# Performance work log

Measured on AMD Instinct MI355X. Metric: run time of the kernel, lower is better.

## Reference

```python
import jax, jax.numpy as jnp
import numpy as np

LN_EPS = 1e-5  # torch LayerNorm default
ITERS = 3

def _ln(x, g, b):
    m = jnp.mean(x, -1, keepdims=True)
    v = jnp.var(x, -1, keepdims=True)
    return (x - m) * jax.lax.rsqrt(v + LN_EPS) * g + b

def setup_inputs() -> dict:
    key = jax.random.key(0)
    ks = jax.random.split(key, 10)
    B, N, D, S, H = 32, 4096, 256, 8, 512
    sc = D ** -0.5
    w = lambda k, shape, s: jax.random.normal(k, shape, jnp.float32) * s
    return {
        "inputs": w(ks[0], (B, N, D), 1.0),
        "noise": w(ks[1], (B, S, D), 1.0),
        "ln_in_g": jnp.ones((D,), jnp.float32), "ln_in_b": jnp.zeros((D,), jnp.float32),
        "ln_slot_g": jnp.ones((D,), jnp.float32), "ln_slot_b": jnp.zeros((D,), jnp.float32),
        "ln_mlp_g": jnp.ones((D,), jnp.float32), "ln_mlp_b": jnp.zeros((D,), jnp.float32),
        "slot_mu": jnp.zeros((1, 1, D), jnp.float32),
        "slot_sigma": jnp.ones((1, 1, D), jnp.float32),
        "Wq": w(ks[2], (D, D), sc), "Wk": w(ks[3], (D, D), sc), "Wv": w(ks[4], (D, D), sc),
        "W_ih": w(ks[5], (D, 3 * D), sc), "W_hh": w(ks[6], (D, 3 * D), sc),
        "b_ih": jnp.zeros((3 * D,), jnp.float32), "b_hh": jnp.zeros((3 * D,), jnp.float32),
        "W1": w(ks[7], (D, H), sc), "b1": jnp.zeros((H,), jnp.float32),
        "W2": w(ks[8], (H, D), H ** -0.5), "b2": jnp.zeros((D,), jnp.float32),
    }

def reference(inputs, noise, ln_in_g, ln_in_b, ln_slot_g, ln_slot_b, ln_mlp_g, ln_mlp_b,
              slot_mu, slot_sigma, Wq, Wk, Wv, W_ih, W_hh, b_ih, b_hh, W1, b1, W2, b2):
    b, n, d = inputs.shape
    scale = d ** -0.5
    x = _ln(inputs, ln_in_g, ln_in_b)
    sigma = jnp.clip(jax.nn.softplus(slot_sigma), 0.1, 2.0)
    slots = slot_mu + sigma * noise            # [b, S, d]
    k = x @ Wk                                  # [b, n, d]
    v = x @ Wv                                  # [b, n, d]
    for _ in range(ITERS):
        slots_prev = slots
        s = _ln(slots, ln_slot_g, ln_slot_b)
        q = s @ Wq                              # [b, S, d]
        dots = jnp.einsum('bnd,bsd->bns', k, q) * scale
        attn = jax.nn.softmax(dots, axis=1)     # softmax over inputs (dim=1), as in source
        updates = jnp.einsum('bns,bnd->bsd', attn, v)
        # torch GRUCell: gate order (reset, update, new)
        gx = updates @ W_ih + b_ih
        gh = slots_prev @ W_hh + b_hh
        xr, xz, xn = jnp.split(gx, 3, -1)
        hr, hz, hn = jnp.split(gh, 3, -1)
        r = jax.nn.sigmoid(xr + hr)
        z = jax.nn.sigmoid(xz + hz)
        ng = jnp.tanh(xn + r * hn)
        slots = (1.0 - z) * ng + z * slots_prev
        m = _ln(slots, ln_mlp_g, ln_mlp_b)
        slots = slots + (jax.nn.relu(m @ W1 + b1) @ W2 + b2)
    return slots
```

## Files before the change

kernel.cpp:

```cpp
#include <hip/hip_runtime.h>

typedef unsigned short u16;
typedef unsigned int u32;
typedef short bf16x8 __attribute__((ext_vector_type(8)));
typedef float f32x4 __attribute__((ext_vector_type(4)));

#define DEV static __device__ __forceinline__

constexpr int CH = 16;
constexpr int NB = 4096 / CH;
constexpr float LN_EPS = 1e-5f;
constexpr float SCALE = 0.0625f;

DEV float bf2f(u32 u) { return __uint_as_float(u << 16); }
DEV float bfe(short x) { return __uint_as_float(((u32)(u16)x) << 16); }
DEV u16 f2bf(float f) {
  u32 u = __float_as_uint(f);
  return (u16)((u + 0x7fffu + ((u >> 16) & 1u)) >> 16);
}
DEV u32 pk2(float a, float b) { return (u32)f2bf(a) | ((u32)f2bf(b) << 16); }


__global__ __launch_bounds__(256) void k_convert(
    const float* __restrict__ Wk, const float* __restrict__ Wv,
    const float* __restrict__ Wih, const float* __restrict__ Whh,
    const float* __restrict__ W1, const float* __restrict__ W2,
    const float* __restrict__ Wq,
    u16* __restrict__ wkvT, u16* __restrict__ wih_f, u16* __restrict__ whh_f,
    u16* __restrict__ w1_f, u16* __restrict__ w2_f, u16* __restrict__ wq_f,
    u16* __restrict__ wqt) {
  int idx = blockIdx.x * 256 + threadIdx.x;
  if (idx < 131072) {
    int n = idx >> 8, k = idx & 255;
    float v = (n < 256) ? Wk[k * 256 + n] : Wv[k * 256 + (n - 256)];
    wkvT[idx] = f2bf(v);
    return;
  }
  idx -= 131072;
  if (idx < 196608) {
    int j = idx & 7, lane = (idx >> 3) & 63, tile = idx >> 9;
    int kt = tile & 7, nt = tile >> 3;
    int k = kt * 32 + ((lane >> 4) << 3) + j, n = nt * 16 + (lane & 15);
    wih_f[idx] = f2bf(Wih[k * 768 + n]);
    return;
  }
  idx -= 196608;
  if (idx < 196608) {
    int j = idx & 7, lane = (idx >> 3) & 63, tile = idx >> 9;
    int kt = tile & 7, nt = tile >> 3;
    int k = kt * 32 + ((lane >> 4) << 3) + j, n = nt * 16 + (lane & 15);
    whh_f[idx] = f2bf(Whh[k * 768 + n]);
    return;
  }
  idx -= 196608;
  if (idx < 131072) {
    int j = idx & 7, lane = (idx >> 3) & 63, tile = idx >> 9;
    int kt = tile & 7, nt = tile >> 3;
    int k = kt * 32 + ((lane >> 4) << 3) + j, n = nt * 16 + (lane & 15);
    w1_f[idx] = f2bf(W1[k * 512 + n]);
    return;
  }
  idx -= 131072;
  if (idx < 131072) {
    int j = idx & 7, lane = (idx >> 3) & 63, tile = idx >> 9;
    int kt = tile & 15, nt = tile >> 4;
    int k = kt * 32 + ((lane >> 4) << 3) + j, n = nt * 16 + (lane & 15);
    w2_f[idx] = f2bf(W2[k * 256 + n]);
    return;
  }
  idx -= 131072;
  if (idx < 65536) {
    int j = idx & 7, lane = (idx >> 3) & 63, tile = idx >> 9;
    int kt = tile & 7, nt = tile >> 3;
    int k = kt * 32 + ((lane >> 4) << 3) + j, n = nt * 16 + (lane & 15);
    wq_f[idx] = f2bf(Wq[k * 256 + n]);
    return;
  }
  idx -= 65536;
  if (idx < 65536) {
    int t = idx >> 8, d = idx & 255;
    wqt[idx] = f2bf(Wq[d * 256 + t]);
    return;
  }
}

__global__ __launch_bounds__(256) void k_ln(const float* __restrict__ in,
    const float* __restrict__ g, const float* __restrict__ b,
    u16* __restrict__ xbf) {
  int row = blockIdx.x * 4 + (threadIdx.x >> 6);
  int lane = threadIdx.x & 63;
  float4 v = ((const float4*)(in + (size_t)row * 256))[lane];
  float s = v.x + v.y + v.z + v.w;
  float ss = v.x * v.x + v.y * v.y + v.z * v.z + v.w * v.w;
#pragma unroll
  for (int o = 32; o; o >>= 1) { s += __shfl_xor(s, o); ss += __shfl_xor(ss, o); }
  float mean = s * (1.f / 256.f);
  float rstd = rsqrtf(ss * (1.f / 256.f) - mean * mean + LN_EPS);
  float4 gv = ((const float4*)g)[lane];
  float4 bv = ((const float4*)b)[lane];
  uint2 o;
  o.x = pk2((v.x - mean) * rstd * gv.x + bv.x, (v.y - mean) * rstd * gv.y + bv.y);
  o.y = pk2((v.z - mean) * rstd * gv.z + bv.z, (v.w - mean) * rstd * gv.w + bv.w);
  ((uint2*)(xbf + (size_t)row * 256))[lane] = o;
}

__global__ __launch_bounds__(256) void k_slots_init(
    const float* __restrict__ noise, const float* __restrict__ mu,
    const float* __restrict__ sig, const float* __restrict__ g,
    const float* __restrict__ b, const u16* __restrict__ wqt,
    float* __restrict__ slots, float* __restrict__ qbuf) {
  int bs = blockIdx.x, t = threadIdx.x;
  float sg = sig[t];
  float sp = (sg > 20.f) ? sg : log1pf(expf(sg));
  sp = fminf(fmaxf(sp, 0.1f), 2.0f);
  float sl = mu[t] + sp * noise[bs * 256 + t];
  slots[bs * 256 + t] = sl;
  __shared__ float red[8];
  __shared__ __align__(16) float sln[256];
  float s = sl, ss = sl * sl;
#pragma unroll
  for (int o = 32; o; o >>= 1) { s += __shfl_xor(s, o); ss += __shfl_xor(ss, o); }
  int w = t >> 6;
  if ((t & 63) == 0) { red[w] = s; red[4 + w] = ss; }
  __syncthreads();
  s = red[0] + red[1] + red[2] + red[3];
  ss = red[4] + red[5] + red[6] + red[7];
  float mean = s * (1.f / 256.f);
  float rstd = rsqrtf(ss * (1.f / 256.f) - mean * mean + LN_EPS);
  sln[t] = (sl - mean) * rstd * g[t] + b[t];
  __syncthreads();
  float acc = 0.f;
  const bf16x8* wqp = (const bf16x8*)(wqt + t * 256);
#pragma unroll 4
  for (int db = 0; db < 32; ++db) {
    float q8[8];
    *(float4*)q8 = *(const float4*)&sln[db * 8];
    *(float4*)(q8 + 4) = *(const float4*)&sln[db * 8 + 4];
    bf16x8 wv = wqp[db];
#pragma unroll
    for (int j = 0; j < 8; ++j) acc += q8[j] * bfe(wv[j]);
  }
  qbuf[bs * 256 + t] = acc;
}

__global__ __launch_bounds__(256) void k_gemm(
    const u16* __restrict__ X, const u16* __restrict__ Wt,
    u16* __restrict__ kT, u16* __restrict__ Vv) {
  __shared__ u16 smem[16896];
  int bid = blockIdx.x;
  int mt = bid >> 2, nt = bid & 3;
  int w = threadIdx.x >> 6, lane = threadIdx.x & 63;
  int wr = w >> 1, wc = w & 1;
  f32x4 acc[4][4] = {};
  for (int ks = 0; ks < 4; ++ks) {
#pragma unroll
    for (int i = 0; i < 4; ++i) {
      int cbase = (w * 4 + i) * 64;
      int c = cbase + lane;
      int r = c >> 3;
      int swz = (c & 7) ^ (r & 7);
      const u16* srcA = X + (mt * 128 + r) * 256 + ks * 64 + swz * 8;
      const u16* srcB = Wt + (nt * 128 + r) * 256 + ks * 64 + swz * 8;
      __builtin_amdgcn_global_load_lds(
          (const __attribute__((address_space(1))) void*)srcA,
          (__attribute__((address_space(3))) void*)(smem + cbase * 8), 16, 0, 0);
      __builtin_amdgcn_global_load_lds(
          (const __attribute__((address_space(1))) void*)srcB,
          (__attribute__((address_space(3))) void*)(smem + 8192 + cbase * 8), 16, 0, 0);
    }
    __syncthreads();
#pragma unroll
    for (int kk = 0; kk < 2; ++kk) {
      bf16x8 af[4], bfr[4];
#pragma unroll
      for (int m = 0; m < 4; ++m) {
        int lrow = wr * 64 + m * 16 + (lane & 15);
        int slot = (kk * 4 + (lane >> 4)) ^ (lrow & 7);
        af[m] = *(const bf16x8*)((const char*)smem + lrow * 128 + slot * 16);
      }
#pragma unroll
      for (int n = 0; n < 4; ++n) {
        int lcol = wc * 64 + n * 16 + (lane & 15);
        int slot = (kk * 4 + (lane >> 4)) ^ (lcol & 7);
        bfr[n] = *(const bf16x8*)((const char*)smem + 16384 + lcol * 128 + slot * 16);
      }
#pragma unroll
      for (int m = 0; m < 4; ++m)
#pragma unroll
        for (int n = 0; n < 4; ++n)
          acc[m][n] = __builtin_amdgcn_mfma_f32_16x16x32_bf16(af[m], bfr[n], acc[m][n], 0, 0, 0);
    }
    __syncthreads();
  }
  int bb = (mt * 128) >> 12;
  int nb0 = (mt * 128) & 4095;
  if (nt < 2) {
#pragma unroll
    for (int m = 0; m < 4; ++m)
#pragma unroll
      for (int n = 0; n < 4; ++n) {
        int col = wc * 64 + n * 16 + (lane & 15);
        int r0 = wr * 64 + m * 16 + (lane >> 4) * 4;
        uint2 pk;
        pk.x = pk2(acc[m][n][0], acc[m][n][1]);
        pk.y = pk2(acc[m][n][2], acc[m][n][3]);
        *(uint2*)((char*)smem + col * 264 + r0 * 2) = pk;
      }
    __syncthreads();
    u16* outp = kT + bb * (1 << 20) + nt * 128 * 4096 + nb0;
    for (int i = 0; i < 32; ++i) {
      int dl = w * 32 + i;
      u32 val = *(const u32*)((const char*)smem + dl * 264 + lane * 4);
      *(u32*)(outp + dl * 4096 + 2 * lane) = val;
    }
  } else {
#pragma unroll
    for (int m = 0; m < 4; ++m)
#pragma unroll
      for (int n = 0; n < 4; ++n) {
        int col = wc * 64 + n * 16 + (lane & 15);
        int r0 = wr * 64 + m * 16 + (lane >> 4) * 4;
#pragma unroll
        for (int j = 0; j < 4; ++j)
          *((u16*)((char*)smem + (r0 + j) * 264 + col * 2)) = f2bf(acc[m][n][j]);
      }
    __syncthreads();
    u16* outp = Vv + (mt * 128) * 256 + (nt - 2) * 128;
    for (int i = 0; i < 32; ++i) {
      int nl = w * 32 + i;
      u32 val = *(const u32*)((const char*)smem + nl * 264 + lane * 4);
      *(u32*)(outp + nl * 256 + 2 * lane) = val;
    }
  }
}

__global__ __launch_bounds__(128) void k_attn(
    const u16* __restrict__ kT, const u16* __restrict__ Vv,
    const float* __restrict__ qbuf,
    float* __restrict__ part_ml, float* __restrict__ part_upd) {
  int b = blockIdx.x >> 4, c = blockIdx.x & 15;
  int n0 = c * NB;
  int t = threadIdx.x;
  int w = t >> 6, lane = t & 63;
  __shared__ __align__(16) float qT[256][8];
  __shared__ __align__(16) float pl[NB][8];
  __shared__ float red[16];
  for (int i = t; i < 2048; i += 128) {
    int s = i >> 8, d = i & 255;
    qT[d][s] = qbuf[(b * 8 + s) * 256 + d];
  }
  __syncthreads();
  float acc[8][2] = {};
  const u16* kp = kT + b * (1 << 20) + n0 + 2 * t;
#pragma unroll 8
  for (int d = 0; d < 256; ++d) {
    u32 kk = *(const u32*)(kp + d * 4096);
    float k0 = bf2f(kk & 0xffffu), k1 = bf2f(kk >> 16);
    float q8[8];
    *(float4*)q8 = *(const float4*)&qT[d][0];
    *(float4*)(q8 + 4) = *(const float4*)&qT[d][4];
#pragma unroll
    for (int s = 0; s < 8; ++s) { acc[s][0] += k0 * q8[s]; acc[s][1] += k1 * q8[s]; }
  }
  float mx[8];
#pragma unroll
  for (int s = 0; s < 8; ++s) {
    acc[s][0] *= SCALE; acc[s][1] *= SCALE;
    float lm = fmaxf(acc[s][0], acc[s][1]);
#pragma unroll
    for (int o = 32; o; o >>= 1) lm = fmaxf(lm, __shfl_xor(lm, o));
    if (lane == 0) red[w * 8 + s] = lm;
  }
  __syncthreads();
#pragma unroll
  for (int s = 0; s < 8; ++s) mx[s] = fmaxf(red[s], red[8 + s]);
  __syncthreads();
#pragma unroll
  for (int s = 0; s < 8; ++s) {
    float p0 = __expf(acc[s][0] - mx[s]);
    float p1 = __expf(acc[s][1] - mx[s]);
    pl[2 * t][s] = p0; pl[2 * t + 1][s] = p1;
    float l = p0 + p1;
#pragma unroll
    for (int o = 32; o; o >>= 1) l += __shfl_xor(l, o);
    if (lane == 0) red[w * 8 + s] = l;
  }
  __syncthreads();
  if (t < 8) {
    part_ml[(b * 16 + c) * 16 + t] = mx[t];
    part_ml[(b * 16 + c) * 16 + 8 + t] = red[t] + red[8 + t];
  }
  float upd[8][2] = {};
  const u16* vp = Vv + (b * 4096 + n0) * 256 + 2 * t;
#pragma unroll 4
  for (int n = 0; n < NB; ++n) {
    u32 vv = *(const u32*)(vp + n * 256);
    float v0 = bf2f(vv & 0xffffu), v1 = bf2f(vv >> 16);
    float p8[8];
    *(float4*)p8 = *(const float4*)&pl[n][0];
    *(float4*)(p8 + 4) = *(const float4*)&pl[n][4];
#pragma unroll
    for (int s = 0; s < 8; ++s) { upd[s][0] += p8[s] * v0; upd[s][1] += p8[s] * v1; }
  }
  float* up = part_upd + ((b * 16 + c) * 8) * 256 + 2 * t;
#pragma unroll
  for (int s = 0; s < 8; ++s) {
    float2 o2; o2.x = upd[s][0]; o2.y = upd[s][1];
    *(float2*)(up + s * 256) = o2;
  }
}

__global__ __launch_bounds__(256) void k_comb(
    const float* __restrict__ pml, const float* __restrict__ pupd,
    const float* __restrict__ slots_in,
    u16* __restrict__ ufrag, u16* __restrict__ hfrag) {
  int w = threadIdx.x >> 6, lane = threadIdx.x & 63;
  int row = blockIdx.x * 4 + w;
  int b = row >> 3, s = row & 7;
  float mv[16], lv[16], M = -1e30f;
#pragma unroll
  for (int c = 0; c < 16; ++c) {
    mv[c] = pml[(b * 16 + c) * 16 + s];
    lv[c] = pml[(b * 16 + c) * 16 + 8 + s];
    M = fmaxf(M, mv[c]);
  }
  float L = 0.f;
#pragma unroll
  for (int c = 0; c < 16; ++c) { mv[c] = __expf(mv[c] - M); L += lv[c] * mv[c]; }
  float inv = 1.f / L;
  int d0 = lane * 4;
  float4 acc = {0.f, 0.f, 0.f, 0.f};
#pragma unroll
  for (int c = 0; c < 16; ++c) {
    float4 p = *(const float4*)(pupd + (size_t)((b * 16 + c) * 8 + s) * 256 + d0);
    float wc = mv[c] * inv;
    acc.x += wc * p.x; acc.y += wc * p.y; acc.z += wc * p.z; acc.w += wc * p.w;
  }
  int mt = row >> 4, kt = d0 >> 5;
  int laneA = ((d0 >> 3) & 3) * 16 + (row & 15);
  int j0 = d0 & 7;
  uint2 pk;
  pk.x = pk2(acc.x, acc.y); pk.y = pk2(acc.z, acc.w);
  *(uint2*)(ufrag + ((mt * 8 + kt) * 64 + laneA) * 8 + j0) = pk;
  float4 hv = *(const float4*)(slots_in + row * 256 + d0);
  pk.x = pk2(hv.x, hv.y); pk.y = pk2(hv.z, hv.w);
  *(uint2*)(hfrag + ((mt * 8 + kt) * 64 + laneA) * 8 + j0) = pk;
}

__global__ __launch_bounds__(256) void k_gru(
    const u16* __restrict__ ufrag, const u16* __restrict__ hfrag,
    const u16* __restrict__ wih_f, const u16* __restrict__ whh_f,
    const float* __restrict__ bih, const float* __restrict__ bhh,
    const float* __restrict__ slots_in, float* __restrict__ snew) {
  int w = threadIdx.x >> 6, lane = threadIdx.x & 63;
  int unit = blockIdx.x * 4 + w;
  int mt = unit >> 4, g = unit & 15;
  const bf16x8* wih = (const bf16x8*)wih_f;
  const bf16x8* whh = (const bf16x8*)whh_f;
  f32x4 ar = {}, az = {}, an = {}, hr = {}, hz = {}, hn = {};
#pragma unroll
  for (int kt = 0; kt < 8; ++kt) {
    bf16x8 au = *(const bf16x8*)(ufrag + ((mt * 8 + kt) * 64 + lane) * 8);
    bf16x8 ah = *(const bf16x8*)(hfrag + ((mt * 8 + kt) * 64 + lane) * 8);
    ar = __builtin_amdgcn_mfma_f32_16x16x32_bf16(au, wih[(g * 8 + kt) * 64 + lane], ar, 0, 0, 0);
    az = __builtin_amdgcn_mfma_f32_16x16x32_bf16(au, wih[((16 + g) * 8 + kt) * 64 + lane], az, 0, 0, 0);
    an = __builtin_amdgcn_mfma_f32_16x16x32_bf16(au, wih[((32 + g) * 8 + kt) * 64 + lane], an, 0, 0, 0);
    hr = __builtin_amdgcn_mfma_f32_16x16x32_bf16(ah, whh[(g * 8 + kt) * 64 + lane], hr, 0, 0, 0);
    hz = __builtin_amdgcn_mfma_f32_16x16x32_bf16(ah, whh[((16 + g) * 8 + kt) * 64 + lane], hz, 0, 0, 0);
    hn = __builtin_amdgcn_mfma_f32_16x16x32_bf16(ah, whh[((32 + g) * 8 + kt) * 64 + lane], hn, 0, 0, 0);
  }
  int t = g * 16 + (lane & 15);
  float cr = bih[t], cz = bih[256 + t], cn = bih[512 + t];
  float dr = bhh[t], dz = bhh[256 + t], dn = bhh[512 + t];
#pragma unroll
  for (int j = 0; j < 4; ++j) {
    int row = mt * 16 + (lane >> 4) * 4 + j;
    float r = 1.f / (1.f + __expf(-(ar[j] + cr + hr[j] + dr)));
    float z = 1.f / (1.f + __expf(-(az[j] + cz + hz[j] + dz)));
    float ng = tanhf(an[j] + cn + r * (hn[j] + dn));
    float h = slots_in[row * 256 + t];
    snew[row * 256 + t] = (1.f - z) * ng + z * h;
  }
}

__global__ __launch_bounds__(256) void k_rowln(
    const float* __restrict__ xin, const float* __restrict__ g,
    const float* __restrict__ bb, u16* __restrict__ frag) {
  int w = threadIdx.x >> 6, lane = threadIdx.x & 63;
  int row = blockIdx.x * 4 + w;
  int d0 = lane * 4;
  float4 v = *(const float4*)(xin + row * 256 + d0);
  float s = v.x + v.y + v.z + v.w;
  float ss = v.x * v.x + v.y * v.y + v.z * v.z + v.w * v.w;
#pragma unroll
  for (int o = 32; o; o >>= 1) { s += __shfl_xor(s, o); ss += __shfl_xor(ss, o); }
  float mean = s * (1.f / 256.f);
  float rstd = rsqrtf(ss * (1.f / 256.f) - mean * mean + LN_EPS);
  float4 gv = *(const float4*)(g + d0);
  float4 bv = *(const float4*)(bb + d0);
  float o0 = (v.x - mean) * rstd * gv.x + bv.x;
  float o1 = (v.y - mean) * rstd * gv.y + bv.y;
  float o2 = (v.z - mean) * rstd * gv.z + bv.z;
  float o3 = (v.w - mean) * rstd * gv.w + bv.w;
  int mt = row >> 4, kt = d0 >> 5;
  int laneA = ((d0 >> 3) & 3) * 16 + (row & 15);
  int j0 = d0 & 7;
  uint2 pk;
  pk.x = pk2(o0, o1); pk.y = pk2(o2, o3);
  *(uint2*)(frag + ((mt * 8 + kt) * 64 + laneA) * 8 + j0) = pk;
}

__global__ __launch_bounds__(256) void k_mlp1(
    const u16* __restrict__ mfrag, const u16* __restrict__ w1_f,
    const float* __restrict__ b1v, u16* __restrict__ h1frag) {
  int w = threadIdx.x >> 6, lane = threadIdx.x & 63;
  int unit = blockIdx.x * 4 + w;
  int mt = unit >> 5, nt = unit & 31;
  const bf16x8* bw = (const bf16x8*)w1_f;
  f32x4 acc = {};
#pragma unroll
  for (int kt = 0; kt < 8; ++kt)
    acc = __builtin_amdgcn_mfma_f32_16x16x32_bf16(
        *(const bf16x8*)(mfrag + ((mt * 8 + kt) * 64 + lane) * 8),
        bw[(nt * 8 + kt) * 64 + lane], acc, 0, 0, 0);
  int col = nt * 16 + (lane & 15);
  float bbv = b1v[col];
  int kt2 = col >> 5;
  int j2 = col & 7;
  int laneBase = ((col >> 3) & 3) * 16;
#pragma unroll
  for (int j = 0; j < 4; ++j) {
    int row = mt * 16 + (lane >> 4) * 4 + j;
    float vv = fmaxf(acc[j] + bbv, 0.f);
    h1frag[((mt * 16 + kt2) * 64 + laneBase + (row & 15)) * 8 + j2] = f2bf(vv);
  }
}

__global__ __launch_bounds__(256) void k_mlp2(
    const u16* __restrict__ h1frag, const u16* __restrict__ w2_f,
    const float* __restrict__ b2v, const float* __restrict__ snew,
    float* __restrict__ sout) {
  int w = threadIdx.x >> 6, lane = threadIdx.x & 63;
  int unit = blockIdx.x * 4 + w;
  int mt = unit >> 4, nt = unit & 15;
  const bf16x8* bw = (const bf16x8*)w2_f;
  f32x4 acc = {};
#pragma unroll
  for (int kt = 0; kt < 16; ++kt)
    acc = __builtin_amdgcn_mfma_f32_16x16x32_bf16(
        *(const bf16x8*)(h1frag + ((mt * 16 + kt) * 64 + lane) * 8),
        bw[(nt * 16 + kt) * 64 + lane], acc, 0, 0, 0);
  int col = nt * 16 + (lane & 15);
  float bbv = b2v[col];
#pragma unroll
  for (int j = 0; j < 4; ++j) {
    int row = mt * 16 + (lane >> 4) * 4 + j;
    sout[row * 256 + col] = acc[j] + bbv + snew[row * 256 + col];
  }
}

__global__ __launch_bounds__(256) void k_q(
    const u16* __restrict__ slfrag, const u16* __restrict__ wq_f,
    float* __restrict__ qbuf) {
  int w = threadIdx.x >> 6, lane = threadIdx.x & 63;
  int unit = blockIdx.x * 4 + w;
  int mt = unit >> 4, nt = unit & 15;
  const bf16x8* bw = (const bf16x8*)wq_f;
  f32x4 acc = {};
#pragma unroll
  for (int kt = 0; kt < 8; ++kt)
    acc = __builtin_amdgcn_mfma_f32_16x16x32_bf16(
        *(const bf16x8*)(slfrag + ((mt * 8 + kt) * 64 + lane) * 8),
        bw[(nt * 8 + kt) * 64 + lane], acc, 0, 0, 0);
  int col = nt * 16 + (lane & 15);
#pragma unroll
  for (int j = 0; j < 4; ++j) {
    int row = mt * 16 + (lane >> 4) * 4 + j;
    qbuf[row * 256 + col] = acc[j];
  }
}

extern "C" void kernel_launch(void* const* d_in, const int* in_sizes, int n_in,
                              void* d_out, int out_size, void* d_ws, size_t ws_size,
                              hipStream_t stream) {
  (void)in_sizes; (void)n_in; (void)out_size; (void)ws_size;
  const float* inputs    = (const float*)d_in[0];
  const float* noise     = (const float*)d_in[1];
  const float* ln_in_g   = (const float*)d_in[2];
  const float* ln_in_b   = (const float*)d_in[3];
  const float* ln_slot_g = (const float*)d_in[4];
  const float* ln_slot_b = (const float*)d_in[5];
  const float* ln_mlp_g  = (const float*)d_in[6];
  const float* ln_mlp_b  = (const float*)d_in[7];
  const float* slot_mu   = (const float*)d_in[8];
  const float* slot_sig  = (const float*)d_in[9];
  const float* Wq        = (const float*)d_in[10];
  const float* Wk        = (const float*)d_in[11];
  const float* Wv        = (const float*)d_in[12];
  const float* W_ih      = (const float*)d_in[13];
  const float* W_hh      = (const float*)d_in[14];
  const float* b_ih      = (const float*)d_in[15];
  const float* b_hh      = (const float*)d_in[16];
  const float* W1        = (const float*)d_in[17];
  const float* b1        = (const float*)d_in[18];
  const float* W2        = (const float*)d_in[19];
  const float* b2        = (const float*)d_in[20];

  char* p = (char*)d_ws;
  auto take = [&](size_t bytes) { char* r = p; p += (bytes + 255) & ~(size_t)255; return r; };
  u16* xbf      = (u16*)take((size_t)131072 * 256 * 2);
  u16* kT       = (u16*)take((size_t)32 * 256 * 4096 * 2);
  u16* Vv       = (u16*)take((size_t)32 * 4096 * 256 * 2);
  u16* wkvT     = (u16*)take(131072 * 2);
  u16* wih_f    = (u16*)take(196608 * 2);
  u16* whh_f    = (u16*)take(196608 * 2);
  u16* w1_f     = (u16*)take(131072 * 2);
  u16* w2_f     = (u16*)take(131072 * 2);
  u16* wq_f     = (u16*)take(65536 * 2);
  u16* wqt      = (u16*)take(65536 * 2);
  u16* ufrag    = (u16*)take(65536 * 2);
  u16* hfrag    = (u16*)take(65536 * 2);
  u16* mfrag    = (u16*)take(65536 * 2);
  u16* slfrag   = (u16*)take(65536 * 2);
  u16* h1frag   = (u16*)take(131072 * 2);
  float* snew   = (float*)take(65536 * 4);
  float* slotsA = (float*)take(256 * 256 * 4);
  float* slotsB = (float*)take(256 * 256 * 4);
  float* qbuf   = (float*)take(256 * 256 * 4);
  float* pml    = (float*)take(32 * 16 * 16 * 4);
  float* pupd   = (float*)take((size_t)32 * 16 * 8 * 256 * 4);

  k_convert<<<3584, 256, 0, stream>>>(Wk, Wv, W_ih, W_hh, W1, W2, Wq,
                                      wkvT, wih_f, whh_f, w1_f, w2_f, wq_f, wqt);
  k_ln<<<32768, 256, 0, stream>>>(inputs, ln_in_g, ln_in_b, xbf);
  k_slots_init<<<256, 256, 0, stream>>>(noise, slot_mu, slot_sig, ln_slot_g, ln_slot_b, wqt, slotsA, qbuf);
  k_gemm<<<4096, 256, 0, stream>>>(xbf, wkvT, kT, Vv);

  const float* scur = slotsA;
  for (int it = 0; it < 3; ++it) {
    k_attn<<<512, 128, 0, stream>>>(kT, Vv, qbuf, pml, pupd);
    k_comb<<<64, 256, 0, stream>>>(pml, pupd, scur, ufrag, hfrag);
    k_gru<<<64, 256, 0, stream>>>(ufrag, hfrag, wih_f, whh_f, b_ih, b_hh, scur, snew);
    k_rowln<<<64, 256, 0, stream>>>(snew, ln_mlp_g, ln_mlp_b, mfrag);
    k_mlp1<<<128, 256, 0, stream>>>(mfrag, w1_f, b1, h1frag);
    float* sout = (it == 2) ? (float*)d_out : ((it == 0) ? slotsB : slotsA);
    k_mlp2<<<64, 256, 0, stream>>>(h1frag, w2_f, b2, snew, sout);
    if (it < 2) {
      k_rowln<<<64, 256, 0, stream>>>(sout, ln_slot_g, ln_slot_b, slfrag);
      k_q<<<64, 256, 0, stream>>>(slfrag, wq_f, qbuf);
    }
    scur = sout;
  }
}
```

Baseline: 324.7 us.

## Fuse LayerNorms into the K/V GEMM, MLP1 and Q projection kernels

The input LayerNorm is computed inside the K/V GEMM. Each block normalizes its 128 fp32 rows straight into swizzled LDS, so the separate k_ln pass and the bf16 xbf buffer in global memory go away. The per-iteration row LayerNorms before MLP1 and the Q projection are likewise folded into those GEMM kernels through shared-memory fragments, which removes four small launches per loop. The trade-offs: the fp32 input is now read once per N-tile (four times per row block), the larger LDS footprint may cut occupancy, and weight tiles are loaded after each barrier with no double buffering.

```diff
diff --git a/kernel.cpp b/kernel.cpp
--- a/kernel.cpp
+++ b/kernel.cpp
@@ -82,26 +82,6 @@
     wqt[idx] = f2bf(Wq[d * 256 + t]);
     return;
   }
-}
-
-__global__ __launch_bounds__(256) void k_ln(const float* __restrict__ in,
-    const float* __restrict__ g, const float* __restrict__ b,
-    u16* __restrict__ xbf) {
-  int row = blockIdx.x * 4 + (threadIdx.x >> 6);
-  int lane = threadIdx.x & 63;
-  float4 v = ((const float4*)(in + (size_t)row * 256))[lane];
-  float s = v.x + v.y + v.z + v.w;
-  float ss = v.x * v.x + v.y * v.y + v.z * v.z + v.w * v.w;
-#pragma unroll
-  for (int o = 32; o; o >>= 1) { s += __shfl_xor(s, o); ss += __shfl_xor(ss, o); }
-  float mean = s * (1.f / 256.f);
-  float rstd = rsqrtf(ss * (1.f / 256.f) - mean * mean + LN_EPS);
-  float4 gv = ((const float4*)g)[lane];
-  float4 bv = ((const float4*)b)[lane];
-  uint2 o;
-  o.x = pk2((v.x - mean) * rstd * gv.x + bv.x, (v.y - mean) * rstd * gv.y + bv.y);
-  o.y = pk2((v.z - mean) * rstd * gv.z + bv.z, (v.w - mean) * rstd * gv.w + bv.w);
-  ((uint2*)(xbf + (size_t)row * 256))[lane] = o;
 }
 
 __global__ __launch_bounds__(256) void k_slots_init(
@@ -143,31 +123,51 @@
   qbuf[bs * 256 + t] = acc;
 }
 
-__global__ __launch_bounds__(256) void k_gemm(
-    const u16* __restrict__ X, const u16* __restrict__ Wt,
+__global__ __launch_bounds__(256) void k_gemm2(
+    const float* __restrict__ inF, const float* __restrict__ lng,
+    const float* __restrict__ lnb, const u16* __restrict__ Wt,
     u16* __restrict__ kT, u16* __restrict__ Vv) {
-  __shared__ u16 smem[16896];
+  __shared__ u16 smem[40960];
   int bid = blockIdx.x;
   int mt = bid >> 2, nt = bid & 3;
   int w = threadIdx.x >> 6, lane = threadIdx.x & 63;
   int wr = w >> 1, wc = w & 1;
+
+  {
+    int ks = 0;
+#pragma unroll
+    for (int i = 0; i < 4; ++i) {
+      int cbase = i * 256 + w * 64;
+      int gi = cbase + lane;
+      int col = gi >> 3, sc = gi & 7;
+      const u16* srcB = Wt + (nt * 128 + col) * 256 + ks * 64 + ((sc ^ (col & 7)) << 3);
+      __builtin_amdgcn_global_load_lds(
+          (const __attribute__((address_space(1))) void*)srcB,
+          (__attribute__((address_space(3))) void*)(smem + 32768 + cbase * 8), 16, 0, 0);
+    }
+  }
+  {
+    float4 gv = ((const float4*)lng)[lane];
+    float4 bv = ((const float4*)lnb)[lane];
+    int cc = lane >> 1, half = lane & 1;
+    for (int i = 0; i < 32; ++i) {
+      int r = w * 32 + i;
+      float4 v = ((const float4*)(inF + (size_t)(mt * 128 + r) * 256))[lane];
+      float s = v.x + v.y + v.z + v.w;
+      float ss = v.x * v.x + v.y * v.y + v.z * v.z + v.w * v.w;
+#pragma unroll
+      for (int o = 32; o; o >>= 1) { s += __shfl_xor(s, o); ss += __shfl_xor(ss, o); }
+      float mean = s * (1.f / 256.f);
+      float rstd = rsqrtf(ss * (1.f / 256.f) - mean * mean + LN_EPS);
+      uint2 pk;
+      pk.x = pk2((v.x - mean) * rstd * gv.x + bv.x, (v.y - mean) * rstd * gv.y + bv.y);
+      pk.y = pk2((v.z - mean) * rstd * gv.z + bv.z, (v.w - mean) * rstd * gv.w + bv.w);
+      int byte = r * 512 + ((cc ^ (r & 7)) << 4) + half * 8;
+      *(uint2*)((char*)smem + byte) = pk;
+    }
+  }
   f32x4 acc[4][4] = {};
   for (int ks = 0; ks < 4; ++ks) {
-#pragma unroll
-    for (int i = 0; i < 4; ++i) {
-      int cbase = (w * 4 + i) * 64;
-      int c = cbase + lane;
-      int r = c >> 3;
-      int swz = (c & 7) ^ (r & 7);
-      const u16* srcA = X + (mt * 128 + r) * 256 + ks * 64 + swz * 8;
-      const u16* srcB = Wt + (nt * 128 + r) * 256 + ks * 64 + swz * 8;
-      __builtin_amdgcn_global_load_lds(
-          (const __attribute__((address_space(1))) void*)srcA,
-          (__attribute__((address_space(3))) void*)(smem + cbase * 8), 16, 0, 0);
-      __builtin_amdgcn_global_load_lds(
-          (const __attribute__((address_space(1))) void*)srcB,
-          (__attribute__((address_space(3))) void*)(smem + 8192 + cbase * 8), 16, 0, 0);
-    }
     __syncthreads();
 #pragma unroll
     for (int kk = 0; kk < 2; ++kk) {
@@ -175,14 +175,14 @@
 #pragma unroll
       for (int m = 0; m < 4; ++m) {
         int lrow = wr * 64 + m * 16 + (lane & 15);
-        int slot = (kk * 4 + (lane >> 4)) ^ (lrow & 7);
-        af[m] = *(const bf16x8*)((const char*)smem + lrow * 128 + slot * 16);
+        int cc = ks * 8 + kk * 4 + (lane >> 4);
+        af[m] = *(const bf16x8*)((const char*)smem + lrow * 512 + ((cc ^ (lrow & 7)) << 4));
       }
 #pragma unroll
       for (int n = 0; n < 4; ++n) {
         int lcol = wc * 64 + n * 16 + (lane & 15);
         int slot = (kk * 4 + (lane >> 4)) ^ (lcol & 7);
-        bfr[n] = *(const bf16x8*)((const char*)smem + 16384 + lcol * 128 + slot * 16);
+        bfr[n] = *(const bf16x8*)((const char*)smem + 65536 + lcol * 128 + slot * 16);
       }
 #pragma unroll
       for (int m = 0; m < 4; ++m)
@@ -191,7 +191,21 @@
           acc[m][n] = __builtin_amdgcn_mfma_f32_16x16x32_bf16(af[m], bfr[n], acc[m][n], 0, 0, 0);
     }
     __syncthreads();
-  }
+    if (ks < 3) {
+      int ks2 = ks + 1;
+#pragma unroll
+      for (int i = 0; i < 4; ++i) {
+        int cbase = i * 256 + w * 64;
+        int gi = cbase + lane;
+        int col = gi >> 3, sc = gi & 7;
+        const u16* srcB = Wt + (nt * 128 + col) * 256 + ks2 * 64 + ((sc ^ (col & 7)) << 3);
+        __builtin_amdgcn_global_load_lds(
+            (const __attribute__((address_space(1))) void*)srcB,
+            (__attribute__((address_space(3))) void*)(smem + 32768 + cbase * 8), 16, 0, 0);
+      }
+    }
+  }
+  __syncthreads();
   int bb = (mt * 128) >> 12;
   int nb0 = (mt * 128) & 4095;
   if (nt < 2) {
@@ -383,56 +397,51 @@
   }
 }
 
-__global__ __launch_bounds__(256) void k_rowln(
-    const float* __restrict__ xin, const float* __restrict__ g,
-    const float* __restrict__ bb, u16* __restrict__ frag) {
+__global__ __launch_bounds__(256) void k_mlp1ln(
+    const float* __restrict__ sn, const float* __restrict__ gm,
+    const float* __restrict__ bm, const u16* __restrict__ w1_f,
+    const float* __restrict__ b1v, u16* __restrict__ h1frag) {
+  __shared__ __align__(16) u16 afr[4096];
   int w = threadIdx.x >> 6, lane = threadIdx.x & 63;
-  int row = blockIdx.x * 4 + w;
+  int mt = blockIdx.x >> 3;
   int d0 = lane * 4;
-  float4 v = *(const float4*)(xin + row * 256 + d0);
-  float s = v.x + v.y + v.z + v.w;
-  float ss = v.x * v.x + v.y * v.y + v.z * v.z + v.w * v.w;
-#pragma unroll
-  for (int o = 32; o; o >>= 1) { s += __shfl_xor(s, o); ss += __shfl_xor(ss, o); }
-  float mean = s * (1.f / 256.f);
-  float rstd = rsqrtf(ss * (1.f / 256.f) - mean * mean + LN_EPS);
-  float4 gv = *(const float4*)(g + d0);
-  float4 bv = *(const float4*)(bb + d0);
-  float o0 = (v.x - mean) * rstd * gv.x + bv.x;
-  float o1 = (v.y - mean) * rstd * gv.y + bv.y;
-  float o2 = (v.z - mean) * rstd * gv.z + bv.z;
-  float o3 = (v.w - mean) * rstd * gv.w + bv.w;
-  int mt = row >> 4, kt = d0 >> 5;
-  int laneA = ((d0 >> 3) & 3) * 16 + (row & 15);
-  int j0 = d0 & 7;
-  uint2 pk;
-  pk.x = pk2(o0, o1); pk.y = pk2(o2, o3);
-  *(uint2*)(frag + ((mt * 8 + kt) * 64 + laneA) * 8 + j0) = pk;
-}
-
-__global__ __launch_bounds__(256) void k_mlp1(
-    const u16* __restrict__ mfrag, const u16* __restrict__ w1_f,
-    const float* __restrict__ b1v, u16* __restrict__ h1frag) {
-  int w = threadIdx.x >> 6, lane = threadIdx.x & 63;
-  int unit = blockIdx.x * 4 + w;
-  int mt = unit >> 5, nt = unit & 31;
+  float4 gvv = *(const float4*)(gm + d0);
+  float4 bvv = *(const float4*)(bm + d0);
+#pragma unroll
+  for (int i = 0; i < 4; ++i) {
+    int r16 = w * 4 + i;
+    float4 v = *(const float4*)(sn + (mt * 16 + r16) * 256 + d0);
+    float s = v.x + v.y + v.z + v.w;
+    float ss = v.x * v.x + v.y * v.y + v.z * v.z + v.w * v.w;
+#pragma unroll
+    for (int o = 32; o; o >>= 1) { s += __shfl_xor(s, o); ss += __shfl_xor(ss, o); }
+    float mean = s * (1.f / 256.f);
+    float rstd = rsqrtf(ss * (1.f / 256.f) - mean * mean + LN_EPS);
+    uint2 pk;
+    pk.x = pk2((v.x - mean) * rstd * gvv.x + bvv.x, (v.y - mean) * rstd * gvv.y + bvv.y);
+    pk.y = pk2((v.z - mean) * rstd * gvv.z + bvv.z, (v.w - mean) * rstd * gvv.w + bvv.w);
+    int kt = lane >> 3;
+    int laneA = ((lane >> 1) & 3) * 16 + r16;
+    *(uint2*)(afr + (kt * 64 + laneA) * 8 + (lane & 1) * 4) = pk;
+  }
+  __syncthreads();
+  int nt = (blockIdx.x & 7) * 4 + w;
   const bf16x8* bw = (const bf16x8*)w1_f;
   f32x4 acc = {};
 #pragma unroll
   for (int kt = 0; kt < 8; ++kt)
     acc = __builtin_amdgcn_mfma_f32_16x16x32_bf16(
-        *(const bf16x8*)(mfrag + ((mt * 8 + kt) * 64 + lane) * 8),
+        *(const bf16x8*)(afr + (kt * 64 + lane) * 8),
         bw[(nt * 8 + kt) * 64 + lane], acc, 0, 0, 0);
   int col = nt * 16 + (lane & 15);
   float bbv = b1v[col];
-  int kt2 = col >> 5;
-  int j2 = col & 7;
+  int kt2 = col >> 5, j2 = col & 7;
   int laneBase = ((col >> 3) & 3) * 16;
 #pragma unroll
   for (int j = 0; j < 4; ++j) {
-    int row = mt * 16 + (lane >> 4) * 4 + j;
+    int r = (lane >> 4) * 4 + j;
     float vv = fmaxf(acc[j] + bbv, 0.f);
-    h1frag[((mt * 16 + kt2) * 64 + laneBase + (row & 15)) * 8 + j2] = f2bf(vv);
+    h1frag[((mt * 16 + kt2) * 64 + laneBase + r) * 8 + j2] = f2bf(vv);
   }
 }
 
@@ -459,18 +468,41 @@
   }
 }
 
-__global__ __launch_bounds__(256) void k_q(
-    const u16* __restrict__ slfrag, const u16* __restrict__ wq_f,
+__global__ __launch_bounds__(256) void k_qln(
+    const float* __restrict__ so, const float* __restrict__ gsv,
+    const float* __restrict__ bsv, const u16* __restrict__ wq_f,
     float* __restrict__ qbuf) {
+  __shared__ __align__(16) u16 afr[4096];
   int w = threadIdx.x >> 6, lane = threadIdx.x & 63;
-  int unit = blockIdx.x * 4 + w;
-  int mt = unit >> 4, nt = unit & 15;
+  int mt = blockIdx.x >> 2;
+  int d0 = lane * 4;
+  float4 gvv = *(const float4*)(gsv + d0);
+  float4 bvv = *(const float4*)(bsv + d0);
+#pragma unroll
+  for (int i = 0; i < 4; ++i) {
+    int r16 = w * 4 + i;
+    float4 v = *(const float4*)(so + (mt * 16 + r16) * 256 + d0);
+    float s = v.x + v.y + v.z + v.w;
+    float ss = v.x * v.x + v.y * v.y + v.z * v.z + v.w * v.w;
+#pragma unroll
+    for (int o = 32; o; o >>= 1) { s += __shfl_xor(s, o); ss += __shfl_xor(ss, o); }
+    float mean = s * (1.f / 256.f);
+    float rstd = rsqrtf(ss * (1.f / 256.f) - mean * mean + LN_EPS);
+    uint2 pk;
+    pk.x = pk2((v.x - mean) * rstd * gvv.x + bvv.x, (v.y - mean) * rstd * gvv.y + bvv.y);
+    pk.y = pk2((v.z - mean) * rstd * gvv.z + bvv.z, (v.w - mean) * rstd * gvv.w + bvv.w);
+    int kt = lane >> 3;
+    int laneA = ((lane >> 1) & 3) * 16 + r16;
+    *(uint2*)(afr + (kt * 64 + laneA) * 8 + (lane & 1) * 4) = pk;
+  }
+  __syncthreads();
+  int nt = (blockIdx.x & 3) * 4 + w;
   const bf16x8* bw = (const bf16x8*)wq_f;
   f32x4 acc = {};
 #pragma unroll
   for (int kt = 0; kt < 8; ++kt)
     acc = __builtin_amdgcn_mfma_f32_16x16x32_bf16(
-        *(const bf16x8*)(slfrag + ((mt * 8 + kt) * 64 + lane) * 8),
+        *(const bf16x8*)(afr + (kt * 64 + lane) * 8),
         bw[(nt * 8 + kt) * 64 + lane], acc, 0, 0, 0);
   int col = nt * 16 + (lane & 15);
 #pragma unroll
@@ -508,7 +540,6 @@
 
   char* p = (char*)d_ws;
   auto take = [&](size_t bytes) { char* r = p; p += (bytes + 255) & ~(size_t)255; return r; };
-  u16* xbf      = (u16*)take((size_t)131072 * 256 * 2);
   u16* kT       = (u16*)take((size_t)32 * 256 * 4096 * 2);
   u16* Vv       = (u16*)take((size_t)32 * 4096 * 256 * 2);
   u16* wkvT     = (u16*)take(131072 * 2);
@@ -520,8 +551,6 @@
   u16* wqt      = (u16*)take(65536 * 2);
   u16* ufrag    = (u16*)take(65536 * 2);
   u16* hfrag    = (u16*)take(65536 * 2);
-  u16* mfrag    = (u16*)take(65536 * 2);
-  u16* slfrag   = (u16*)take(65536 * 2);
   u16* h1frag   = (u16*)take(131072 * 2);
   float* snew   = (float*)take(65536 * 4);
   float* slotsA = (float*)take(256 * 256 * 4);
@@ -532,23 +561,18 @@
 
   k_convert<<<3584, 256, 0, stream>>>(Wk, Wv, W_ih, W_hh, W1, W2, Wq,
                                       wkvT, wih_f, whh_f, w1_f, w2_f, wq_f, wqt);
-  k_ln<<<32768, 256, 0, stream>>>(inputs, ln_in_g, ln_in_b, xbf);
   k_slots_init<<<256, 256, 0, stream>>>(noise, slot_mu, slot_sig, ln_slot_g, ln_slot_b, wqt, slotsA, qbuf);
-  k_gemm<<<4096, 256, 0, stream>>>(xbf, wkvT, kT, Vv);
+  k_gemm2<<<4096, 256, 0, stream>>>(inputs, ln_in_g, ln_in_b, wkvT, kT, Vv);
 
   const float* scur = slotsA;
   for (int it = 0; it < 3; ++it) {
     k_attn<<<512, 128, 0, stream>>>(kT, Vv, qbuf, pml, pupd);
     k_comb<<<64, 256, 0, stream>>>(pml, pupd, scur, ufrag, hfrag);
     k_gru<<<64, 256, 0, stream>>>(ufrag, hfrag, wih_f, whh_f, b_ih, b_hh, scur, snew);
-    k_rowln<<<64, 256, 0, stream>>>(snew, ln_mlp_g, ln_mlp_b, mfrag);
-    k_mlp1<<<128, 256, 0, stream>>>(mfrag, w1_f, b1, h1frag);
+    k_mlp1ln<<<128, 256, 0, stream>>>(snew, ln_mlp_g, ln_mlp_b, w1_f, b1, h1frag);
     float* sout = (it == 2) ? (float*)d_out : ((it == 0) ? slotsB : slotsA);
     k_mlp2<<<64, 256, 0, stream>>>(h1frag, w2_f, b2, snew, sout);
-    if (it < 2) {
-      k_rowln<<<64, 256, 0, stream>>>(sout, ln_slot_g, ln_slot_b, slfrag);
-      k_q<<<64, 256, 0, stream>>>(slfrag, wq_f, qbuf);
-    }
+    if (it < 2) k_qln<<<64, 256, 0, stream>>>(sout, ln_slot_g, ln_slot_b, wq_f, qbuf);
     scur = sout;
   }
 }
```

Result: slower. 467.4 us (+44.0%).
